# Kernel optimization log

Measured on AMD Instinct MI355X. Metric: run time of the kernel, lower is better.

The kernel has to match this reference:

```python
import jax, jax.numpy as jnp
import numpy as np

B, T, D_ENC, V, E, H = 16, 2000, 512, 1024, 256, 2
P, J = 640, 640
BLANK = 0


def _lin(k, i, o):
    s = 1.0 / np.sqrt(i)
    return jax.random.uniform(k, (i, o), jnp.float32, -s, s)


def setup_inputs() -> dict:
    key = jax.random.key(0)
    ks = jax.random.split(key, 12)
    return {
        "encoder_out": jax.random.normal(ks[0], (B, T, D_ENC), jnp.float32),
        "features_len": jnp.full((B,), T, jnp.int32),
        "targets": jax.random.randint(ks[1], (B, T), 0, V),
        "W_enc": _lin(ks[2], D_ENC, V), "b_enc": jnp.zeros((V,), jnp.float32),
        "emb": jax.random.normal(ks[3], (V, E), jnp.float32) * 0.1,
        "W_p1": _lin(ks[4], H * E, P), "b_p1": jnp.zeros((P,), jnp.float32),
        "W_p2": _lin(ks[5], P, P), "b_p2": jnp.zeros((P,), jnp.float32),
        "W_po": _lin(ks[6], P, V), "b_po": jnp.zeros((V,), jnp.float32),
        "W_j1": _lin(ks[7], V, J), "b_j1": jnp.zeros((J,), jnp.float32),
        "W_j2": _lin(ks[8], J, V), "b_j2": jnp.zeros((V,), jnp.float32),
    }


def _viterbi_context(targets):
    # c[0] = blank; c[t] = targets[t-1] if targets[t-1] != blank else c[t-1]
    # == last non-blank target at a position strictly before t, else blank.
    t_idx = jnp.arange(targets.shape[1])
    pos = jnp.where(targets != BLANK, t_idx[None, :], -1)
    last = jax.lax.cummax(pos, axis=1)                                   # [B,T] last non-blank idx <= t
    last = jnp.pad(last[:, :-1], ((0, 0), (1, 0)), constant_values=-1)   # strictly < t
    gathered = jnp.take_along_axis(targets, jnp.maximum(last, 0), axis=1)
    return jnp.where(last >= 0, gathered, BLANK)


def _extend_context_history(context):
    # stack [c, shift(c,1), ...] along last dim, padding with blank
    hist = [context]
    for _ in range(H - 1):
        hist.append(jnp.pad(hist[-1][:, :-1], ((0, 0), (1, 0)), constant_values=BLANK))
    return jnp.stack(hist, axis=-1)  # [B,T,H]


def reference(encoder_out, features_len, targets, W_enc, b_enc, emb,
              W_p1, b_p1, W_p2, b_p2, W_po, b_po, W_j1, b_j1, W_j2, b_j2):
    # encoder head
    enc = encoder_out @ W_enc + b_enc                    # [B,T,V]
    enc_lens = features_len.astype(jnp.int32)
    enc_log_probs = jax.nn.log_softmax(enc, axis=2)

    # viterbi context + predictor (dropout is identity in eval/reference)
    ctx = _extend_context_history(_viterbi_context(targets))   # [B,T,H]
    a = emb[ctx]                                                # [B,T,H,E]
    a = a.reshape(*a.shape[:-2], H * E)                         # [B,T,H*E]
    a = jnp.tanh(a @ W_p1 + b_p1)
    a = jnp.tanh(a @ W_p2 + b_p2)
    pred = a @ W_po + b_po                                      # [B,T,V]
    pred_log_probs = jax.nn.log_softmax(pred, axis=2)

    # joint network on enc + pred
    h = jnp.tanh((enc + pred) @ W_j1 + b_j1)
    logits = h @ W_j2 + b_j2
    log_probs = jax.nn.log_softmax(logits, axis=2)
    return log_probs, pred_log_probs, enc_log_probs, enc_lens
```

## Files before the change

kernel.cpp:

```cpp
#include <hip/hip_runtime.h>
#include <math.h>

typedef unsigned short ushort_t;
typedef unsigned int uint_t;

#define BB 16
#define TT 2000
#define DENC 512
#define VV 1024
#define EE 256
#define PP 640
#define MM (BB * TT)

typedef __attribute__((ext_vector_type(8))) short bf16x8;
typedef __attribute__((ext_vector_type(4))) float f32x4;

__device__ __forceinline__ ushort_t f2bf(float x) {
    union { float f; uint_t u; } v; v.f = x;
    uint_t r = v.u + 0x7fffu + ((v.u >> 16) & 1u);
    return (ushort_t)(r >> 16);
}

__device__ __forceinline__ void async_ld16(const ushort_t* g, ushort_t* l) {
    __builtin_amdgcn_global_load_lds(
        (const __attribute__((address_space(1))) void*)g,
        (__attribute__((address_space(3))) void*)l, 16, 0, 0);
}

__global__ void ctx_kernel(const int* __restrict__ targets,
                           int* __restrict__ ctx0, int* __restrict__ ctx1) {
    __shared__ int tg[TT];
    __shared__ int cc[TT];
    const int b = blockIdx.x;
    const int* row = targets + b * TT;
    for (int t = threadIdx.x; t < TT; t += blockDim.x) tg[t] = row[t];
    __syncthreads();
    if (threadIdx.x == 0) {
        int cur = 0;
        for (int t = 0; t < TT; ++t) {
            cc[t] = cur;
            int v = tg[t];
            cur = (v != 0) ? v : cur;
        }
    }
    __syncthreads();
    for (int t = threadIdx.x; t < TT; t += blockDim.x) {
        ctx0[b * TT + t] = cc[t];
        ctx1[b * TT + t] = (t >= 1) ? cc[t - 1] : 0;
    }
}

__global__ __launch_bounds__(256) void transpose_cvt_kernel(
    const float* __restrict__ W, ushort_t* __restrict__ WT, int K, int N) {
    __shared__ float t[32][33];
    const int n0 = blockIdx.x * 32, k0 = blockIdx.y * 32;
    const int tx = threadIdx.x, ty0 = threadIdx.y;
    #pragma unroll
    for (int i = 0; i < 4; ++i) {
        int ty = ty0 + i * 8;
        t[ty][tx] = W[(size_t)(k0 + ty) * N + n0 + tx];
    }
    __syncthreads();
    #pragma unroll
    for (int i = 0; i < 4; ++i) {
        int ty = ty0 + i * 8;
        WT[(size_t)(n0 + ty) * K + k0 + tx] = f2bf(t[tx][ty]);
    }
}

__global__ __launch_bounds__(256) void cvt_kernel(const float* __restrict__ in,
                                                  ushort_t* __restrict__ out, int n) {
    int i = (blockIdx.x * 256 + threadIdx.x) * 4;
    if (i >= n) return;
    float4 v = *(const float4*)(in + i);
    ushort_t o[4] = {f2bf(v.x), f2bf(v.y), f2bf(v.z), f2bf(v.w)};
    *(uint2*)(out + i) = *(uint2*)o;
}

__global__ __launch_bounds__(128) void gather_kernel(const float* __restrict__ emb,
                                                     const int* __restrict__ ctx0,
                                                     const int* __restrict__ ctx1,
                                                     ushort_t* __restrict__ out) {
    const int m = blockIdx.x;
    const int t = threadIdx.x;
    const int half = t >> 6;
    const int c = half ? ctx1[m] : ctx0[m];
    const int e = (t & 63) * 4;
    float4 v = *(const float4*)&emb[(size_t)c * EE + e];
    ushort_t o[4] = {f2bf(v.x), f2bf(v.y), f2bf(v.z), f2bf(v.w)};
    *(uint2*)&out[(size_t)m * 512 + half * 256 + e] = *(uint2*)o;
}

template<bool TANH, bool OUTBF, bool SUM>
__global__ __launch_bounds__(256) void gemm_bf16_kernel(
    const ushort_t* __restrict__ A, const ushort_t* __restrict__ BT,
    const float* __restrict__ bias, void* __restrict__ Cout,
    const float* __restrict__ addIn, ushort_t* __restrict__ sumOut,
    int M, int N, int K, int GX) {
    __shared__ __align__(16) ushort_t As[128 * 32];
    __shared__ __align__(16) ushort_t Bs[128 * 32];

    const int nwg = gridDim.x;
    const int orig = blockIdx.x;
    const int q = nwg >> 3, r = nwg & 7;
    const int xcd = orig & 7, slot = orig >> 3;
    const int wgid = (xcd < r ? xcd * (q + 1) : r * (q + 1) + (xcd - r) * q) + slot;
    const int bx = wgid % GX, by = wgid / GX;

    const int tid = threadIdx.x;
    const int wave = tid >> 6, lane = tid & 63;
    const int ln = lane & 15, quad = lane >> 4;
    const int wr = wave >> 1, wc = wave & 1;
    const int rowBase = by * 128;
    const int colBase = bx * 128;

    const int c0 = wave * 64 + lane;
    const int r0 = c0 >> 2, ko0 = (c0 & 3) * 8;
    const int c1 = 256 + c0;
    const int r1 = c1 >> 2, ko1 = (c1 & 3) * 8;
    const ushort_t* gA0 = A + (size_t)(rowBase + r0) * K + ko0;
    const ushort_t* gA1 = A + (size_t)(rowBase + r1) * K + ko1;
    const ushort_t* gB0 = BT + (size_t)(colBase + r0) * K + ko0;
    const ushort_t* gB1 = BT + (size_t)(colBase + r1) * K + ko1;
    ushort_t* lA0 = As + wave * 512;
    ushort_t* lA1 = As + 2048 + wave * 512;
    ushort_t* lB0 = Bs + wave * 512;
    ushort_t* lB1 = Bs + 2048 + wave * 512;

    f32x4 acc[4][4] = {};

    for (int k0 = 0; k0 < K; k0 += 32) {
        async_ld16(gA0 + k0, lA0);
        async_ld16(gA1 + k0, lA1);
        async_ld16(gB0 + k0, lB0);
        async_ld16(gB1 + k0, lB1);
        __syncthreads();

        bf16x8 a[4], b[4];
        #pragma unroll
        for (int i = 0; i < 4; ++i)
            a[i] = *(const bf16x8*)&As[(wr * 64 + i * 16 + ln) * 32 + quad * 8];
        #pragma unroll
        for (int j = 0; j < 4; ++j)
            b[j] = *(const bf16x8*)&Bs[(wc * 64 + j * 16 + ln) * 32 + quad * 8];
        #pragma unroll
        for (int i = 0; i < 4; ++i)
            #pragma unroll
            for (int j = 0; j < 4; ++j)
                acc[i][j] = __builtin_amdgcn_mfma_f32_16x16x32_bf16(a[i], b[j], acc[i][j], 0, 0, 0);
        __syncthreads();
    }

    float bv[4];
    #pragma unroll
    for (int j = 0; j < 4; ++j) bv[j] = bias[colBase + wc * 64 + j * 16 + ln];

    #pragma unroll
    for (int i = 0; i < 4; ++i) {
        #pragma unroll
        for (int rr = 0; rr < 4; ++rr) {
            const size_t row = (size_t)(rowBase + wr * 64 + i * 16 + quad * 4 + rr);
            #pragma unroll
            for (int j = 0; j < 4; ++j) {
                const int col = colBase + wc * 64 + j * 16 + ln;
                const size_t idx = row * (size_t)N + col;
                float v = acc[i][j][rr] + bv[j];
                if (TANH) v = tanhf(v);
                if (SUM) {
                    ((float*)Cout)[idx] = v;
                    sumOut[idx] = f2bf(v + addIn[idx]);
                } else if (OUTBF) {
                    ((ushort_t*)Cout)[idx] = f2bf(v);
                } else {
                    ((float*)Cout)[idx] = v;
                }
            }
        }
    }
}

__device__ __forceinline__ void stage_half(const ushort_t* __restrict__ X, int xBase,
                                           int K, int kt, int h, ushort_t* region,
                                           int tid) {
    const int wb = tid & ~63;
    #pragma unroll
    for (int s = 0; s < 2; ++s) {
        const int c  = s * 512 + tid;
        const int rH = c >> 3;
        const int k8 = (c & 7) ^ (rH & 7);
        const ushort_t* g = X + (size_t)(xBase + h * 128 + rH) * K + kt + k8 * 8;
        ushort_t* l = region + ((size_t)(h * 1024 + s * 512 + wb)) * 8;
        async_ld16(g, l);
    }
}

template<bool SUM>
__global__ __launch_bounds__(512, 2) void gemm256_kernel(
    const ushort_t* __restrict__ A, const ushort_t* __restrict__ BT,
    const float* __restrict__ bias, float* __restrict__ Cout,
    const float* __restrict__ addIn, ushort_t* __restrict__ sumOut,
    int M, int N, int K, int GX) {
    extern __shared__ __align__(16) ushort_t sm[];
    ushort_t* A0 = sm;
    ushort_t* B0 = sm + 16384;
    ushort_t* A1 = sm + 32768;
    ushort_t* B1 = sm + 49152;

    const int nwg = gridDim.x;
    const int orig = blockIdx.x;
    const int q8 = nwg >> 3, r8 = nwg & 7;
    const int xcd = orig & 7, slot = orig >> 3;
    const int wgid = (xcd < r8 ? xcd * (q8 + 1) : r8 * (q8 + 1) + (xcd - r8) * q8) + slot;
    const int bx = wgid % GX, by = wgid / GX;

    const int tid = threadIdx.x;
    const int lane = tid & 63;
    const int ln = lane & 15, quad = lane >> 4;
    const int wave = tid >> 6;
    const int wr = wave >> 2, wc = wave & 3;
    const int rowBase = by * 256, colBase = bx * 256;
    const int NT = K >> 6;

    f32x4 acc[4][2][4] = {};

    stage_half(A,  rowBase, K, 0,  0, A0, tid);
    stage_half(A,  rowBase, K, 0,  1, A0, tid);
    stage_half(BT, colBase, K, 0,  0, B0, tid);
    stage_half(BT, colBase, K, 0,  1, B0, tid);
    stage_half(BT, colBase, K, 64, 0, B1, tid);
    stage_half(BT, colBase, K, 64, 1, B1, tid);
    asm volatile("s_waitcnt vmcnt(4)" ::: "memory");
    __builtin_amdgcn_s_barrier();

    for (int t = 0; t < NT; ++t) {
        const int cur = t & 1;
        const char* cA = (const char*)(cur ? A1 : A0);
        const char* cB = (const char*)(cur ? B1 : B0);
        ushort_t* oA = cur ? A0 : A1;
        ushort_t* cBw = cur ? B1 : B0;
        const int ktA = (t + 1 < NT ? t + 1 : NT - 1) * 64;
        const int ktB = (t + 2 < NT ? t + 2 : NT - 1) * 64;

        bf16x8 bfr[4][2];
        #pragma unroll
        for (int q = 0; q < 4; ++q) {
            if (q == 0) {
                #pragma unroll
                for (int n = 0; n < 4; ++n)
                    #pragma unroll
                    for (int ks = 0; ks < 2; ++ks) {
                        int off = (wc * 64 + n * 16 + ln) * 128 + ks * 64 + quad * 16;
                        off ^= (ln & 7) << 4;
                        bfr[n][ks] = *(const bf16x8*)(cB + off);
                    }
            }
            bf16x8 afr[2][2];
            #pragma unroll
            for (int m = 0; m < 2; ++m)
                #pragma unroll
                for (int ks = 0; ks < 2; ++ks) {
                    int off = (wr * 128 + q * 32 + m * 16 + ln) * 128 + ks * 64 + quad * 16;
                    off ^= (ln & 7) << 4;
                    afr[m][ks] = *(const bf16x8*)(cA + off);
                }
            if (q == 0)      stage_half(A,  rowBase, K, ktA, 0, oA, tid);
            else if (q == 1) stage_half(A,  rowBase, K, ktA, 1, oA, tid);
            else if (q == 2) stage_half(BT, colBase, K, ktB, 0, cBw, tid);
            else             stage_half(BT, colBase, K, ktB, 1, cBw, tid);

            __builtin_amdgcn_s_barrier();
            __builtin_amdgcn_s_setprio(1);
            #pragma unroll
            for (int m = 0; m < 2; ++m)
                #pragma unroll
                for (int n = 0; n < 4; ++n)
                    #pragma unroll
                    for (int ks = 0; ks < 2; ++ks)
                        acc[q][m][n] = __builtin_amdgcn_mfma_f32_16x16x32_bf16(
                            afr[m][ks], bfr[n][ks], acc[q][m][n], 0, 0, 0);
            __builtin_amdgcn_s_setprio(0);
            if (q == 3)
                asm volatile("s_waitcnt vmcnt(4)" ::: "memory");
            __builtin_amdgcn_s_barrier();
        }
    }

    float bv[4];
    #pragma unroll
    for (int n = 0; n < 4; ++n) bv[n] = bias[colBase + wc * 64 + n * 16 + ln];

    #pragma unroll
    for (int q = 0; q < 4; ++q)
        #pragma unroll
        for (int m = 0; m < 2; ++m)
            #pragma unroll
            for (int rr = 0; rr < 4; ++rr) {
                const size_t row = (size_t)(rowBase + wr * 128 + q * 32 + m * 16 + quad * 4 + rr);
                #pragma unroll
                for (int n = 0; n < 4; ++n) {
                    const int col = colBase + wc * 64 + n * 16 + ln;
                    const size_t idx = row * (size_t)N + col;
                    float v = acc[q][m][n][rr] + bv[n];
                    Cout[idx] = v;
                    if (SUM) sumOut[idx] = f2bf(v + addIn[idx]);
                }
            }
}

__global__ __launch_bounds__(256) void logsoftmax_kernel(float* __restrict__ x) {
    const int wave = threadIdx.x >> 6, lane = threadIdx.x & 63;
    const size_t base = ((size_t)blockIdx.x * 4 + wave) * VV;

    float4 v[4];
    #pragma unroll
    for (int i = 0; i < 4; ++i)
        v[i] = *(const float4*)&x[base + i * 256 + lane * 4];

    float m = fmaxf(fmaxf(v[0].x, v[0].y), fmaxf(v[0].z, v[0].w));
    #pragma unroll
    for (int i = 1; i < 4; ++i)
        m = fmaxf(m, fmaxf(fmaxf(v[i].x, v[i].y), fmaxf(v[i].z, v[i].w)));
    #pragma unroll
    for (int o = 1; o < 64; o <<= 1) m = fmaxf(m, __shfl_xor(m, o, 64));

    float s = 0.f;
    #pragma unroll
    for (int i = 0; i < 4; ++i)
        s += expf(v[i].x - m) + expf(v[i].y - m) + expf(v[i].z - m) + expf(v[i].w - m);
    #pragma unroll
    for (int o = 1; o < 64; o <<= 1) s += __shfl_xor(s, o, 64);

    const float lse = logf(s) + m;
    #pragma unroll
    for (int i = 0; i < 4; ++i) {
        v[i].x -= lse; v[i].y -= lse; v[i].z -= lse; v[i].w -= lse;
        *(float4*)&x[base + i * 256 + lane * 4] = v[i];
    }
}

__global__ void lens_kernel(const int* __restrict__ features_len,
                            float* __restrict__ out_lens) {
    if (threadIdx.x < BB) out_lens[threadIdx.x] = (float)features_len[threadIdx.x];
}

extern "C" void kernel_launch(void* const* d_in, const int* in_sizes, int n_in,
                              void* d_out, int out_size, void* d_ws, size_t ws_size,
                              hipStream_t stream) {
    const float* encoder_out  = (const float*)d_in[0];
    const int*   features_len = (const int*)  d_in[1];
    const int*   targets      = (const int*)  d_in[2];
    const float* W_enc = (const float*)d_in[3];
    const float* b_enc = (const float*)d_in[4];
    const float* emb   = (const float*)d_in[5];
    const float* W_p1  = (const float*)d_in[6];
    const float* b_p1  = (const float*)d_in[7];
    const float* W_p2  = (const float*)d_in[8];
    const float* b_p2  = (const float*)d_in[9];
    const float* W_po  = (const float*)d_in[10];
    const float* b_po  = (const float*)d_in[11];
    const float* W_j1  = (const float*)d_in[12];
    const float* b_j1  = (const float*)d_in[13];
    const float* W_j2  = (const float*)d_in[14];
    const float* b_j2  = (const float*)d_in[15];

    float* out = (float*)d_out;
    const size_t BTV = (size_t)MM * VV;
    float* out_logits = out;
    float* out_pred   = out + BTV;
    float* out_enc    = out + 2 * BTV;
    float* out_lens   = out + 3 * BTV;

    char* ws = (char*)d_ws;
    int*      ctx0   = (int*)ws;
    int*      ctx1   = (int*)(ws + 128000);
    size_t off = 256000;
    ushort_t* WTenc = (ushort_t*)(ws + off); off += (size_t)VV * DENC * 2;
    ushort_t* WTp1  = (ushort_t*)(ws + off); off += (size_t)PP * DENC * 2;
    ushort_t* WTp2  = (ushort_t*)(ws + off); off += (size_t)PP * PP * 2;
    ushort_t* WTpo  = (ushort_t*)(ws + off); off += (size_t)VV * PP * 2;
    ushort_t* WTj1  = (ushort_t*)(ws + off); off += (size_t)PP * VV * 2;
    ushort_t* WTj2  = (ushort_t*)(ws + off); off += (size_t)VV * PP * 2;
    ushort_t* h1    = (ushort_t*)(ws + off);
    ushort_t* Abuf  = (ushort_t*)(ws + off + (size_t)MM * PP * 2);
    ushort_t* h2    = (ushort_t*)(ws + off + (size_t)MM * PP * 2
                                          + (size_t)MM * DENC * 2);
    ushort_t* sumb  = h1;

    hipFuncSetAttribute((const void*)&gemm256_kernel<false>,
                        hipFuncAttributeMaxDynamicSharedMemorySize, 131072);
    hipFuncSetAttribute((const void*)&gemm256_kernel<true>,
                        hipFuncAttributeMaxDynamicSharedMemorySize, 131072);

    ctx_kernel<<<BB, 256, 0, stream>>>(targets, ctx0, ctx1);

    dim3 tcb(32, 8);
    transpose_cvt_kernel<<<dim3(VV/32, DENC/32), tcb, 0, stream>>>(W_enc, WTenc, DENC, VV);
    transpose_cvt_kernel<<<dim3(PP/32, DENC/32), tcb, 0, stream>>>(W_p1, WTp1, DENC, PP);
    transpose_cvt_kernel<<<dim3(PP/32, PP/32),   tcb, 0, stream>>>(W_p2, WTp2, PP, PP);
    transpose_cvt_kernel<<<dim3(VV/32, PP/32),   tcb, 0, stream>>>(W_po, WTpo, PP, VV);
    transpose_cvt_kernel<<<dim3(PP/32, VV/32),   tcb, 0, stream>>>(W_j1, WTj1, VV, PP);
    transpose_cvt_kernel<<<dim3(VV/32, PP/32),   tcb, 0, stream>>>(W_j2, WTj2, PP, VV);

    gather_kernel<<<MM, 128, 0, stream>>>(emb, ctx0, ctx1, Abuf);
    gemm_bf16_kernel<true, true, false><<<(PP/128)*(MM/128), 256, 0, stream>>>(
        Abuf, WTp1, b_p1, h1, nullptr, nullptr, MM, PP, DENC, PP/128);

    cvt_kernel<<<(MM * DENC / 4 + 255) / 256, 256, 0, stream>>>(encoder_out, Abuf, MM * DENC);
    gemm256_kernel<false><<<(VV/256)*(MM/256), 512, 131072, stream>>>(
        Abuf, WTenc, b_enc, out_enc, nullptr, nullptr, MM, VV, DENC, VV/256);

    gemm_bf16_kernel<true, true, false><<<(PP/128)*(MM/128), 256, 0, stream>>>(
        h1, WTp2, b_p2, h2, nullptr, nullptr, MM, PP, PP, PP/128);

    gemm256_kernel<true><<<(VV/256)*(MM/256), 512, 131072, stream>>>(
        h2, WTpo, b_po, out_pred, out_enc, sumb, MM, VV, PP, VV/256);

    gemm_bf16_kernel<true, true, false><<<(PP/128)*(MM/128), 256, 0, stream>>>(
        sumb, WTj1, b_j1, h2, nullptr, nullptr, MM, PP, VV, PP/128);

    gemm256_kernel<false><<<(VV/256)*(MM/256), 512, 131072, stream>>>(
        h2, WTj2, b_j2, out_logits, nullptr, nullptr, MM, VV, PP, VV/256);

    logsoftmax_kernel<<<3 * MM / 4, 256, 0, stream>>>(out);

    lens_kernel<<<1, 64, 0, stream>>>(features_len, out_lens);
}
```

Measured before the change: 969.5 us.

## Fuse prep kernels, pad P GEMMs to 768, gather embeddings inside GEMM

All preprocessing (encoder bf16 conversion, weight transposes, embedding conversion, zero padding, bias padding, context scan, lens) is merged into one multi-role prep kernel, and the context scan becomes a parallel max-scan. The N=640 GEMMs move from the 128-tile kernel to the 256-tile pipelined kernel by padding P to 768, with tanh+bf16 output as a new mode. The first predictor GEMM gathers embedding rows directly through ctx indices, so the separate gather pass is removed. This trades launch overhead and weaker tiles for about 20% extra padded FLOPs on the P-sized GEMMs.

```diff
diff --git a/kernel.cpp b/kernel.cpp
--- a/kernel.cpp
+++ b/kernel.cpp
@@ -10,6 +10,7 @@
 #define VV 1024
 #define EE 256
 #define PP 640
+#define PPAD 768
 #define MM (BB * TT)
 
 typedef __attribute__((ext_vector_type(8))) short bf16x8;
@@ -27,160 +28,140 @@
         (__attribute__((address_space(3))) void*)l, 16, 0, 0);
 }
 
-__global__ void ctx_kernel(const int* __restrict__ targets,
-                           int* __restrict__ ctx0, int* __restrict__ ctx1) {
-    __shared__ int tg[TT];
-    __shared__ int cc[TT];
-    const int b = blockIdx.x;
-    const int* row = targets + b * TT;
-    for (int t = threadIdx.x; t < TT; t += blockDim.x) tg[t] = row[t];
-    __syncthreads();
-    if (threadIdx.x == 0) {
-        int cur = 0;
-        for (int t = 0; t < TT; ++t) {
-            cc[t] = cur;
-            int v = tg[t];
-            cur = (v != 0) ? v : cur;
-        }
-    }
-    __syncthreads();
-    for (int t = threadIdx.x; t < TT; t += blockDim.x) {
-        ctx0[b * TT + t] = cc[t];
-        ctx1[b * TT + t] = (t >= 1) ? cc[t - 1] : 0;
-    }
-}
-
-__global__ __launch_bounds__(256) void transpose_cvt_kernel(
-    const float* __restrict__ W, ushort_t* __restrict__ WT, int K, int N) {
-    __shared__ float t[32][33];
-    const int n0 = blockIdx.x * 32, k0 = blockIdx.y * 32;
-    const int tx = threadIdx.x, ty0 = threadIdx.y;
-    #pragma unroll
-    for (int i = 0; i < 4; ++i) {
-        int ty = ty0 + i * 8;
-        t[ty][tx] = W[(size_t)(k0 + ty) * N + n0 + tx];
-    }
-    __syncthreads();
-    #pragma unroll
-    for (int i = 0; i < 4; ++i) {
-        int ty = ty0 + i * 8;
-        WT[(size_t)(n0 + ty) * K + k0 + tx] = f2bf(t[tx][ty]);
-    }
-}
-
-__global__ __launch_bounds__(256) void cvt_kernel(const float* __restrict__ in,
-                                                  ushort_t* __restrict__ out, int n) {
-    int i = (blockIdx.x * 256 + threadIdx.x) * 4;
-    if (i >= n) return;
-    float4 v = *(const float4*)(in + i);
-    ushort_t o[4] = {f2bf(v.x), f2bf(v.y), f2bf(v.z), f2bf(v.w)};
-    *(uint2*)(out + i) = *(uint2*)o;
-}
-
-__global__ __launch_bounds__(128) void gather_kernel(const float* __restrict__ emb,
-                                                     const int* __restrict__ ctx0,
-                                                     const int* __restrict__ ctx1,
-                                                     ushort_t* __restrict__ out) {
-    const int m = blockIdx.x;
-    const int t = threadIdx.x;
-    const int half = t >> 6;
-    const int c = half ? ctx1[m] : ctx0[m];
-    const int e = (t & 63) * 4;
-    float4 v = *(const float4*)&emb[(size_t)c * EE + e];
-    ushort_t o[4] = {f2bf(v.x), f2bf(v.y), f2bf(v.z), f2bf(v.w)};
-    *(uint2*)&out[(size_t)m * 512 + half * 256 + e] = *(uint2*)o;
-}
-
-template<bool TANH, bool OUTBF, bool SUM>
-__global__ __launch_bounds__(256) void gemm_bf16_kernel(
-    const ushort_t* __restrict__ A, const ushort_t* __restrict__ BT,
-    const float* __restrict__ bias, void* __restrict__ Cout,
-    const float* __restrict__ addIn, ushort_t* __restrict__ sumOut,
-    int M, int N, int K, int GX) {
-    __shared__ __align__(16) ushort_t As[128 * 32];
-    __shared__ __align__(16) ushort_t Bs[128 * 32];
-
-    const int nwg = gridDim.x;
-    const int orig = blockIdx.x;
-    const int q = nwg >> 3, r = nwg & 7;
-    const int xcd = orig & 7, slot = orig >> 3;
-    const int wgid = (xcd < r ? xcd * (q + 1) : r * (q + 1) + (xcd - r) * q) + slot;
-    const int bx = wgid % GX, by = wgid / GX;
-
+#define NB_CVT  16000
+#define B_TR    16000
+#define NB_TR   3152
+#define B_EMB   (B_TR + NB_TR)
+#define NB_EMB  256
+#define B_PAD   (B_EMB + NB_EMB)
+#define NB_PAD  34
+#define B_MISC  (B_PAD + NB_PAD)
+#define B_CTX   (B_MISC + 1)
+#define NB_PREP (B_CTX + BB)
+
+__global__ __launch_bounds__(256) void prep_kernel(
+    const float* __restrict__ encoder_out, const int* __restrict__ features_len,
+    const int* __restrict__ targets,
+    const float* __restrict__ W_enc, const float* __restrict__ W_p1,
+    const float* __restrict__ W_p2,  const float* __restrict__ W_po,
+    const float* __restrict__ W_j1,  const float* __restrict__ W_j2,
+    const float* __restrict__ b_p1,  const float* __restrict__ b_p2,
+    const float* __restrict__ b_j1,  const float* __restrict__ emb,
+    ushort_t* __restrict__ Abuf,
+    ushort_t* __restrict__ WTenc, ushort_t* __restrict__ WTp1,
+    ushort_t* __restrict__ WTp2,  ushort_t* __restrict__ WTpo,
+    ushort_t* __restrict__ WTj1,  ushort_t* __restrict__ WTj2,
+    ushort_t* __restrict__ embB,
+    float* __restrict__ bp1p, float* __restrict__ bp2p, float* __restrict__ bj1p,
+    int* __restrict__ ctx0, int* __restrict__ ctx1, float* __restrict__ out_lens) {
+    const int blk = blockIdx.x;
     const int tid = threadIdx.x;
-    const int wave = tid >> 6, lane = tid & 63;
-    const int ln = lane & 15, quad = lane >> 4;
-    const int wr = wave >> 1, wc = wave & 1;
-    const int rowBase = by * 128;
-    const int colBase = bx * 128;
-
-    const int c0 = wave * 64 + lane;
-    const int r0 = c0 >> 2, ko0 = (c0 & 3) * 8;
-    const int c1 = 256 + c0;
-    const int r1 = c1 >> 2, ko1 = (c1 & 3) * 8;
-    const ushort_t* gA0 = A + (size_t)(rowBase + r0) * K + ko0;
-    const ushort_t* gA1 = A + (size_t)(rowBase + r1) * K + ko1;
-    const ushort_t* gB0 = BT + (size_t)(colBase + r0) * K + ko0;
-    const ushort_t* gB1 = BT + (size_t)(colBase + r1) * K + ko1;
-    ushort_t* lA0 = As + wave * 512;
-    ushort_t* lA1 = As + 2048 + wave * 512;
-    ushort_t* lB0 = Bs + wave * 512;
-    ushort_t* lB1 = Bs + 2048 + wave * 512;
-
-    f32x4 acc[4][4] = {};
-
-    for (int k0 = 0; k0 < K; k0 += 32) {
-        async_ld16(gA0 + k0, lA0);
-        async_ld16(gA1 + k0, lA1);
-        async_ld16(gB0 + k0, lB0);
-        async_ld16(gB1 + k0, lB1);
+
+    if (blk < NB_CVT) {
+        size_t i = ((size_t)blk * 256 + tid) * 4;
+        float4 v = *(const float4*)(encoder_out + i);
+        ushort_t o[4] = {f2bf(v.x), f2bf(v.y), f2bf(v.z), f2bf(v.w)};
+        *(uint2*)(Abuf + i) = *(uint2*)o;
+        return;
+    }
+    if (blk < B_EMB) {
+        int t = blk - B_TR;
+        const float* W; ushort_t* WT; int K, N, base;
+        if (t < 512)       { W = W_enc; WT = WTenc; K = 512;  N = 1024; base = 0; }
+        else if (t < 832)  { W = W_p1;  WT = WTp1;  K = 512;  N = 640;  base = 512; }
+        else if (t < 1232) { W = W_p2;  WT = WTp2;  K = 640;  N = 640;  base = 832; }
+        else if (t < 1872) { W = W_po;  WT = WTpo;  K = 640;  N = 1024; base = 1232; }
+        else if (t < 2512) { W = W_j1;  WT = WTj1;  K = 1024; N = 640;  base = 1872; }
+        else               { W = W_j2;  WT = WTj2;  K = 640;  N = 1024; base = 2512; }
+        t -= base;
+        const int tilesN = N / 32;
+        const int n0 = (t % tilesN) * 32, k0 = (t / tilesN) * 32;
+        __shared__ float sm[32][33];
+        const int tx = tid & 31, ty0 = tid >> 5;
+        #pragma unroll
+        for (int i = 0; i < 4; ++i) {
+            int ty = ty0 + i * 8;
+            sm[ty][tx] = W[(size_t)(k0 + ty) * N + n0 + tx];
+        }
         __syncthreads();
-
-        bf16x8 a[4], b[4];
-        #pragma unroll
-        for (int i = 0; i < 4; ++i)
-            a[i] = *(const bf16x8*)&As[(wr * 64 + i * 16 + ln) * 32 + quad * 8];
-        #pragma unroll
-        for (int j = 0; j < 4; ++j)
-            b[j] = *(const bf16x8*)&Bs[(wc * 64 + j * 16 + ln) * 32 + quad * 8];
-        #pragma unroll
-        for (int i = 0; i < 4; ++i)
-            #pragma unroll
-            for (int j = 0; j < 4; ++j)
-                acc[i][j] = __builtin_amdgcn_mfma_f32_16x16x32_bf16(a[i], b[j], acc[i][j], 0, 0, 0);
+        #pragma unroll
+        for (int i = 0; i < 4; ++i) {
+            int ty = ty0 + i * 8;
+            WT[(size_t)(n0 + ty) * K + k0 + tx] = f2bf(sm[tx][ty]);
+        }
+        return;
+    }
+    if (blk < B_PAD) {
+        int t = blk - B_EMB;
+        size_t i = ((size_t)t * 256 + tid) * 4;
+        float4 v = *(const float4*)(emb + i);
+        ushort_t o[4] = {f2bf(v.x), f2bf(v.y), f2bf(v.z), f2bf(v.w)};
+        *(uint2*)(embB + i) = *(uint2*)o;
+        return;
+    }
+    if (blk < B_MISC) {
+        int t = blk - B_PAD;
+        ushort_t* dst; size_t off;
+        if (t < 8)       { dst = WTp1 + (size_t)640 * 512;  off = (size_t)t * 8192; }
+        else if (t < 18) { dst = WTp2 + (size_t)640 * 640;  off = (size_t)(t - 8) * 8192; }
+        else             { dst = WTj1 + (size_t)640 * 1024; off = (size_t)(t - 18) * 8192; }
+        uint4 z = {0, 0, 0, 0};
+        ushort_t* p = dst + off + tid * 32;
+        #pragma unroll
+        for (int i = 0; i < 4; ++i) *(uint4*)(p + i * 8) = z;
+        return;
+    }
+    if (blk < B_CTX) {
+        for (int t = tid; t < PPAD; t += 256) {
+            bp1p[t] = (t < PP) ? b_p1[t] : 0.f;
+            bp2p[t] = (t < PP) ? b_p2[t] : 0.f;
+            bj1p[t] = (t < PP) ? b_j1[t] : 0.f;
+        }
+        if (tid < BB) out_lens[tid] = (float)features_len[tid];
+        return;
+    }
+    {
+        const int b = blk - B_CTX;
+        __shared__ int tg[2048];
+        __shared__ int cc[2048];
+        __shared__ int wl[4];
+        const int* row = targets + b * TT;
+        for (int t = tid; t < 2048; t += 256) tg[t] = (t < TT) ? row[t] : 0;
         __syncthreads();
-    }
-
-    float bv[4];
-    #pragma unroll
-    for (int j = 0; j < 4; ++j) bv[j] = bias[colBase + wc * 64 + j * 16 + ln];
-
-    #pragma unroll
-    for (int i = 0; i < 4; ++i) {
-        #pragma unroll
-        for (int rr = 0; rr < 4; ++rr) {
-            const size_t row = (size_t)(rowBase + wr * 64 + i * 16 + quad * 4 + rr);
-            #pragma unroll
-            for (int j = 0; j < 4; ++j) {
-                const int col = colBase + wc * 64 + j * 16 + ln;
-                const size_t idx = row * (size_t)N + col;
-                float v = acc[i][j][rr] + bv[j];
-                if (TANH) v = tanhf(v);
-                if (SUM) {
-                    ((float*)Cout)[idx] = v;
-                    sumOut[idx] = f2bf(v + addIn[idx]);
-                } else if (OUTBF) {
-                    ((ushort_t*)Cout)[idx] = f2bf(v);
-                } else {
-                    ((float*)Cout)[idx] = v;
-                }
-            }
+        const int lane = tid & 63, wv = tid >> 6;
+        const int base = tid * 8;
+        int lastIdx = -1;
+        #pragma unroll
+        for (int i = 0; i < 8; ++i) { if (tg[base + i] != 0) lastIdx = base + i; }
+        int incl = lastIdx;
+        #pragma unroll
+        for (int o = 1; o < 64; o <<= 1) {
+            int u = __shfl_up(incl, o, 64);
+            if (lane >= o) incl = max(incl, u);
+        }
+        if (lane == 63) wl[wv] = incl;
+        __syncthreads();
+        int excl = -1;
+        for (int w = 0; w < 4; ++w) if (w < wv) excl = max(excl, wl[w]);
+        int u = __shfl_up(incl, 1, 64);
+        if (lane > 0) excl = max(excl, u);
+        int cur = excl;
+        #pragma unroll
+        for (int i = 0; i < 8; ++i) {
+            int idx = base + i;
+            cc[idx] = (cur >= 0) ? tg[cur] : 0;
+            if (tg[idx] != 0) cur = idx;
+        }
+        __syncthreads();
+        for (int t = tid; t < TT; t += 256) {
+            ctx0[b * TT + t] = cc[t];
+            ctx1[b * TT + t] = t ? cc[t - 1] : 0;
         }
     }
 }
 
 __device__ __forceinline__ void stage_half(const ushort_t* __restrict__ X, int xBase,
-                                           int K, int kt, int h, ushort_t* region,
+                                           int lda, int kt, int h, ushort_t* region,
                                            int tid) {
     const int wb = tid & ~63;
     #pragma unroll
@@ -188,23 +169,35 @@
         const int c  = s * 512 + tid;
         const int rH = c >> 3;
         const int k8 = (c & 7) ^ (rH & 7);
-        const ushort_t* g = X + (size_t)(xBase + h * 128 + rH) * K + kt + k8 * 8;
+        const ushort_t* g = X + (size_t)(xBase + h * 128 + rH) * lda + kt + k8 * 8;
         ushort_t* l = region + ((size_t)(h * 1024 + s * 512 + wb)) * 8;
         async_ld16(g, l);
     }
 }
 
-template<bool SUM>
+__device__ __forceinline__ void stage_g(const ushort_t* b0, const ushort_t* b1,
+                                        int kt, int h, int s, ushort_t* region, int tid) {
+    const int wb = tid & ~63;
+    const int c  = s * 512 + tid;
+    const int rH = c >> 3;
+    const int k8 = (c & 7) ^ (rH & 7);
+    const ushort_t* base = (kt < 256) ? (b0 + kt) : (b1 + (kt - 256));
+    async_ld16(base + k8 * 8, region + ((size_t)(h * 1024 + s * 512 + wb)) * 8);
+}
+
+template<int OMODE, bool GATHER>
 __global__ __launch_bounds__(512, 2) void gemm256_kernel(
     const ushort_t* __restrict__ A, const ushort_t* __restrict__ BT,
-    const float* __restrict__ bias, float* __restrict__ Cout,
+    const float* __restrict__ bias, void* __restrict__ Cout,
     const float* __restrict__ addIn, ushort_t* __restrict__ sumOut,
-    int M, int N, int K, int GX) {
-    extern __shared__ __align__(16) ushort_t sm[];
-    ushort_t* A0 = sm;
-    ushort_t* B0 = sm + 16384;
-    ushort_t* A1 = sm + 32768;
-    ushort_t* B1 = sm + 49152;
+    const ushort_t* __restrict__ embB, const int* __restrict__ ctx0,
+    const int* __restrict__ ctx1,
+    int N, int K, int lda, int ldc, int GX) {
+    extern __shared__ __align__(16) ushort_t smem[];
+    ushort_t* A0 = smem;
+    ushort_t* B0 = smem + 16384;
+    ushort_t* A1 = smem + 32768;
+    ushort_t* B1 = smem + 49152;
 
     const int nwg = gridDim.x;
     const int orig = blockIdx.x;
@@ -221,10 +214,31 @@
     const int rowBase = by * 256, colBase = bx * 256;
     const int NT = K >> 6;
 
+    const ushort_t* g0[2][2];
+    const ushort_t* g1[2][2];
+    if (GATHER) {
+        #pragma unroll
+        for (int h = 0; h < 2; ++h)
+            #pragma unroll
+            for (int s = 0; s < 2; ++s) {
+                int rH = (s * 512 + tid) >> 3;
+                int row = rowBase + h * 128 + rH;
+                g0[h][s] = embB + (size_t)ctx0[row] * EE;
+                g1[h][s] = embB + (size_t)ctx1[row] * EE;
+            }
+    }
+
     f32x4 acc[4][2][4] = {};
 
-    stage_half(A,  rowBase, K, 0,  0, A0, tid);
-    stage_half(A,  rowBase, K, 0,  1, A0, tid);
+    if (GATHER) {
+        stage_g(g0[0][0], g1[0][0], 0, 0, 0, A0, tid);
+        stage_g(g0[0][1], g1[0][1], 0, 0, 1, A0, tid);
+        stage_g(g0[1][0], g1[1][0], 0, 1, 0, A0, tid);
+        stage_g(g0[1][1], g1[1][1], 0, 1, 1, A0, tid);
+    } else {
+        stage_half(A, rowBase, lda, 0, 0, A0, tid);
+        stage_half(A, rowBase, lda, 0, 1, A0, tid);
+    }
     stage_half(BT, colBase, K, 0,  0, B0, tid);
     stage_half(BT, colBase, K, 0,  1, B0, tid);
     stage_half(BT, colBase, K, 64, 0, B1, tid);
@@ -236,7 +250,7 @@
         const int cur = t & 1;
         const char* cA = (const char*)(cur ? A1 : A0);
         const char* cB = (const char*)(cur ? B1 : B0);
-        ushort_t* oA = cur ? A0 : A1;
+        ushort_t* oA  = cur ? A0 : A1;
         ushort_t* cBw = cur ? B1 : B0;
         const int ktA = (t + 1 < NT ? t + 1 : NT - 1) * 64;
         const int ktB = (t + 2 < NT ? t + 2 : NT - 1) * 64;
@@ -263,10 +277,19 @@
                     off ^= (ln & 7) << 4;
                     afr[m][ks] = *(const bf16x8*)(cA + off);
                 }
-            if (q == 0)      stage_half(A,  rowBase, K, ktA, 0, oA, tid);
-            else if (q == 1) stage_half(A,  rowBase, K, ktA, 1, oA, tid);
-            else if (q == 2) stage_half(BT, colBase, K, ktB, 0, cBw, tid);
-            else             stage_half(BT, colBase, K, ktB, 1, cBw, tid);
+            if (q == 0) {
+                if (GATHER) { stage_g(g0[0][0], g1[0][0], ktA, 0, 0, oA, tid);
+                              stage_g(g0[0][1], g1[0][1], ktA, 0, 1, oA, tid); }
+                else        stage_half(A, rowBase, lda, ktA, 0, oA, tid);
+            } else if (q == 1) {
+                if (GATHER) { stage_g(g0[1][0], g1[1][0], ktA, 1, 0, oA, tid);
+                              stage_g(g0[1][1], g1[1][1], ktA, 1, 1, oA, tid); }
+                else        stage_half(A, rowBase, lda, ktA, 1, oA, tid);
+            } else if (q == 2) {
+                stage_half(BT, colBase, K, ktB, 0, cBw, tid);
+            } else {
+                stage_half(BT, colBase, K, ktB, 1, cBw, tid);
+            }
 
             __builtin_amdgcn_s_barrier();
             __builtin_amdgcn_s_setprio(1);
@@ -299,10 +322,16 @@
                 #pragma unroll
                 for (int n = 0; n < 4; ++n) {
                     const int col = colBase + wc * 64 + n * 16 + ln;
-                    const size_t idx = row * (size_t)N + col;
+                    const size_t idx = row * (size_t)ldc + col;
                     float v = acc[q][m][n][rr] + bv[n];
-                    Cout[idx] = v;
-                    if (SUM) sumOut[idx] = f2bf(v + addIn[idx]);
+                    if (OMODE == 0) {
+                        ((float*)Cout)[idx] = v;
+                    } else if (OMODE == 1) {
+                        ((ushort_t*)Cout)[idx] = f2bf(tanhf(v));
+                    } else {
+                        ((float*)Cout)[idx] = v;
+                        sumOut[idx] = f2bf(v + addIn[idx]);
+                    }
                 }
             }
 }
@@ -336,11 +365,6 @@
         v[i].x -= lse; v[i].y -= lse; v[i].z -= lse; v[i].w -= lse;
         *(float4*)&x[base + i * 256 + lane * 4] = v[i];
     }
-}
-
-__global__ void lens_kernel(const int* __restrict__ features_len,
-                            float* __restrict__ out_lens) {
-    if (threadIdx.x < BB) out_lens[threadIdx.x] = (float)features_len[threadIdx.x];
 }
 
 extern "C" void kernel_launch(void* const* d_in, const int* in_sizes, int n_in,
@@ -371,57 +395,63 @@
     float* out_lens   = out + 3 * BTV;
 
     char* ws = (char*)d_ws;
-    int*      ctx0   = (int*)ws;
-    int*      ctx1   = (int*)(ws + 128000);
+    int*      ctx0  = (int*)ws;
+    int*      ctx1  = (int*)(ws + 128000);
     size_t off = 256000;
+    ushort_t* embB  = (ushort_t*)(ws + off); off += (size_t)VV * EE * 2;
     ushort_t* WTenc = (ushort_t*)(ws + off); off += (size_t)VV * DENC * 2;
-    ushort_t* WTp1  = (ushort_t*)(ws + off); off += (size_t)PP * DENC * 2;
-    ushort_t* WTp2  = (ushort_t*)(ws + off); off += (size_t)PP * PP * 2;
+    ushort_t* WTp1  = (ushort_t*)(ws + off); off += (size_t)PPAD * DENC * 2;
+    ushort_t* WTp2  = (ushort_t*)(ws + off); off += (size_t)PPAD * PP * 2;
     ushort_t* WTpo  = (ushort_t*)(ws + off); off += (size_t)VV * PP * 2;
-    ushort_t* WTj1  = (ushort_t*)(ws + off); off += (size_t)PP * VV * 2;
+    ushort_t* WTj1  = (ushort_t*)(ws + off); off += (size_t)PPAD * VV * 2;
     ushort_t* WTj2  = (ushort_t*)(ws + off); off += (size_t)VV * PP * 2;
-    ushort_t* h1    = (ushort_t*)(ws + off);
-    ushort_t* Abuf  = (ushort_t*)(ws + off + (size_t)MM * PP * 2);
-    ushort_t* h2    = (ushort_t*)(ws + off + (size_t)MM * PP * 2
-                                          + (size_t)MM * DENC * 2);
+    float*    bp1p  = (float*)(ws + off); off += PPAD * 4;
+    float*    bp2p  = (float*)(ws + off); off += PPAD * 4;
+    float*    bj1p  = (float*)(ws + off); off += PPAD * 4;
+    ushort_t* h1    = (ushort_t*)(ws + off); off += (size_t)MM * PPAD * 2;
+    ushort_t* Abuf  = (ushort_t*)(ws + off); off += (size_t)MM * DENC * 2;
+    ushort_t* h2    = (ushort_t*)(ws + off);
     ushort_t* sumb  = h1;
 
-    hipFuncSetAttribute((const void*)&gemm256_kernel<false>,
+    hipFuncSetAttribute((const void*)&gemm256_kernel<1, true>,
                         hipFuncAttributeMaxDynamicSharedMemorySize, 131072);
-    hipFuncSetAttribute((const void*)&gemm256_kernel<true>,
+    hipFuncSetAttribute((const void*)&gemm256_kernel<0, false>,
                         hipFuncAttributeMaxDynamicSharedMemorySize, 131072);
-
-    ctx_kernel<<<BB, 256, 0, stream>>>(targets, ctx0, ctx1);
-
-    dim3 tcb(32, 8);
-    transpose_cvt_kernel<<<dim3(VV/32, DENC/32), tcb, 0, stream>>>(W_enc, WTenc, DENC, VV);
-    transpose_cvt_kernel<<<dim3(PP/32, DENC/32), tcb, 0, stream>>>(W_p1, WTp1, DENC, PP);
-    transpose_cvt_kernel<<<dim3(PP/32, PP/32),   tcb, 0, stream>>>(W_p2, WTp2, PP, PP);
-    transpose_cvt_kernel<<<dim3(VV/32, PP/32),   tcb, 0, stream>>>(W_po, WTpo, PP, VV);
-    transpose_cvt_kernel<<<dim3(PP/32, VV/32),   tcb, 0, stream>>>(W_j1, WTj1, VV, PP);
-    transpose_cvt_kernel<<<dim3(VV/32, PP/32),   tcb, 0, stream>>>(W_j2, WTj2, PP, VV);
-
-    gather_kernel<<<MM, 128, 0, stream>>>(emb, ctx0, ctx1, Abuf);
-    gemm_bf16_kernel<true, true, false><<<(PP/128)*(MM/128), 256, 0, stream>>>(
-        Abuf, WTp1, b_p1, h1, nullptr, nullptr, MM, PP, DENC, PP/128);
-
-    cvt_kernel<<<(MM * DENC / 4 + 255) / 256, 256, 0, stream>>>(encoder_out, Abuf, MM * DENC);
-    gemm256_kernel<false><<<(VV/256)*(MM/256), 512, 131072, stream>>>(
-        Abuf, WTenc, b_enc, out_enc, nullptr, nullptr, MM, VV, DENC, VV/256);
-
-    gemm_bf16_kernel<true, true, false><<<(PP/128)*(MM/128), 256, 0, stream>>>(
-        h1, WTp2, b_p2, h2, nullptr, nullptr, MM, PP, PP, PP/128);
-
-    gemm256_kernel<true><<<(VV/256)*(MM/256), 512, 131072, stream>>>(
-        h2, WTpo, b_po, out_pred, out_enc, sumb, MM, VV, PP, VV/256);
-
-    gemm_bf16_kernel<true, true, false><<<(PP/128)*(MM/128), 256, 0, stream>>>(
-        sumb, WTj1, b_j1, h2, nullptr, nullptr, MM, PP, VV, PP/128);
-
-    gemm256_kernel<false><<<(VV/256)*(MM/256), 512, 131072, stream>>>(
-        h2, WTj2, b_j2, out_logits, nullptr, nullptr, MM, VV, PP, VV/256);
+    hipFuncSetAttribute((const void*)&gemm256_kernel<1, false>,
+                        hipFuncAttributeMaxDynamicSharedMemorySize, 131072);
+    hipFuncSetAttribute((const void*)&gemm256_kernel<2, false>,
+                        hipFuncAttributeMaxDynamicSharedMemorySize, 131072);
+
+    prep_kernel<<<NB_PREP, 256, 0, stream>>>(
+        encoder_out, features_len, targets,
+        W_enc, W_p1, W_p2, W_po, W_j1, W_j2,
+        b_p1, b_p2, b_j1, emb,
+        Abuf, WTenc, WTp1, WTp2, WTpo, WTj1, WTj2,
+        embB, bp1p, bp2p, bj1p, ctx0, ctx1, out_lens);
+
+    gemm256_kernel<1, true><<<(PPAD/256)*(MM/256), 512, 131072, stream>>>(
+        nullptr, WTp1, bp1p, h1, nullptr, nullptr, embB, ctx0, ctx1,
+        PPAD, DENC, 0, PPAD, PPAD/256);
+
+    gemm256_kernel<0, false><<<(VV/256)*(MM/256), 512, 131072, stream>>>(
+        Abuf, WTenc, b_enc, out_enc, nullptr, nullptr, nullptr, nullptr, nullptr,
+        VV, DENC, DENC, VV, VV/256);
+
+    gemm256_kernel<1, false><<<(PPAD/256)*(MM/256), 512, 131072, stream>>>(
+        h1, WTp2, bp2p, h2, nullptr, nullptr, nullptr, nullptr, nullptr,
+        PPAD, PP, PPAD, PPAD, PPAD/256);
+
+    gemm256_kernel<2, false><<<(VV/256)*(MM/256), 512, 131072, stream>>>(
+        h2, WTpo, b_po, out_pred, out_enc, sumb, nullptr, nullptr, nullptr,
+        VV, PP, PPAD, VV, VV/256);
+
+    gemm256_kernel<1, false><<<(PPAD/256)*(MM/256), 512, 131072, stream>>>(
+        sumb, WTj1, bj1p, h2, nullptr, nullptr, nullptr, nullptr, nullptr,
+        PPAD, VV, VV, PPAD, PPAD/256);
+
+    gemm256_kernel<0, false><<<(VV/256)*(MM/256), 512, 131072, stream>>>(
+        h2, WTj2, b_j2, out_logits, nullptr, nullptr, nullptr, nullptr, nullptr,
+        VV, PP, PPAD, VV, VV/256);
 
     logsoftmax_kernel<<<3 * MM / 4, 256, 0, stream>>>(out);
-
-    lens_kernel<<<1, 64, 0, stream>>>(features_len, out_lens);
-}
+}
```

Measured after the change: 952.4 us. No clear change (-1.8%).
